# Kernel optimization log

Hardware: AMD Instinct MI355X
Metric: run time of the kernel (lower is better)

Reference implementation:

```python
import jax, jax.numpy as jnp
import numpy as np

N = 100000      # nodes
E = 1600000     # edges (avg degree 16)
IN = 128
HID = 128
HEADS = 4
OUT = 64
NEG_SLOPE = 0.2  # PyG GATv2Conv default


def _normal(key, shape, scale=0.05):
    return scale * jax.random.normal(key, shape, dtype=jnp.float32)


def setup_inputs() -> dict:
    key = jax.random.key(0)
    ks = jax.random.split(key, 20)
    x = jax.random.normal(ks[0], (N, IN), dtype=jnp.float32)
    # edges guaranteed non-self-loop (PyG removes then re-adds self loops)
    src = jax.random.randint(ks[1], (E,), 0, N)
    off = jax.random.randint(ks[2], (E,), 1, N)
    dst = (src + off) % N
    edge_index = jnp.stack([src, dst]).astype(jnp.int64)
    C1 = HID // HEADS  # 32 per head
    return {
        "x": x,
        "edge_index": edge_index,
        # layer 1: GATv2Conv(IN -> C1, heads=HEADS, concat=True)
        "Wl1": _normal(ks[3], (IN, HEADS * C1)), "bl1": jnp.zeros((HEADS * C1,), jnp.float32),
        "Wr1": _normal(ks[4], (IN, HEADS * C1)), "br1": jnp.zeros((HEADS * C1,), jnp.float32),
        "att1": _normal(ks[5], (HEADS, C1)),
        "b1": jnp.zeros((HEADS * C1,), jnp.float32),
        # layer 2: GATv2Conv(HID -> HID, heads=1, concat=False)
        "Wl2": _normal(ks[6], (HID, HID)), "bl2": jnp.zeros((HID,), jnp.float32),
        "Wr2": _normal(ks[7], (HID, HID)), "br2": jnp.zeros((HID,), jnp.float32),
        "att2": _normal(ks[8], (1, HID)),
        "b2": jnp.zeros((HID,), jnp.float32),
        # residual skips
        "skip1_w": _normal(ks[9], (IN, HID)), "skip1_b": jnp.zeros((HID,), jnp.float32),
        "skip2_w": _normal(ks[10], (HID, HID)), "skip2_b": jnp.zeros((HID,), jnp.float32),
        # MLP head
        "mlp1_w": _normal(ks[11], (HID, HID)), "mlp1_b": jnp.zeros((HID,), jnp.float32),
        "mlp2_w": _normal(ks[12], (HID, OUT)), "mlp2_b": jnp.zeros((OUT,), jnp.float32),
    }


def gatv2_layer(x, src, dst, Wl, bl, Wr, br, att, bias, heads, outc, concat, n):
    # x: [n, F]; src/dst: [Etot] (self-loops included)
    xl = (x @ Wl + bl).reshape(n, heads, outc)  # source transform
    xr = (x @ Wr + br).reshape(n, heads, outc)  # target transform
    e = jax.nn.leaky_relu(xl[src] + xr[dst], NEG_SLOPE)   # [Etot, H, C]
    logits = jnp.einsum('ehc,hc->eh', e, att)             # [Etot, H]
    # segment softmax over incoming edges of each target node
    m = jax.ops.segment_max(logits, dst, num_segments=n)
    a = jnp.exp(logits - m[dst])
    denom = jax.ops.segment_sum(a, dst, num_segments=n)
    alpha = a / denom[dst]                                # [Etot, H]
    msg = alpha[:, :, None] * xl[src]                     # [Etot, H, C]
    out = jax.ops.segment_sum(msg, dst, num_segments=n)   # [n, H, C]
    out = out.reshape(n, heads * outc) if concat else out.mean(axis=1)
    return out + bias


def reference(x, edge_index, Wl1, bl1, Wr1, br1, att1, b1,
              Wl2, bl2, Wr2, br2, att2, b2,
              skip1_w, skip1_b, skip2_w, skip2_b,
              mlp1_w, mlp1_b, mlp2_w, mlp2_b):
    n = x.shape[0]
    loop = jnp.arange(n, dtype=edge_index.dtype)
    src = jnp.concatenate([edge_index[0], loop])
    dst = jnp.concatenate([edge_index[1], loop])
    # layer 0 + skip + relu (dropout off: eval mode)
    h = gatv2_layer(x, src, dst, Wl1, bl1, Wr1, br1, att1, b1,
                    HEADS, HID // HEADS, True, n)
    h = jax.nn.relu(h + x @ skip1_w + skip1_b)
    # final conv layer (heads=1, concat=False) + skip
    h2 = gatv2_layer(h, src, dst, Wl2, bl2, Wr2, br2, att2, b2,
                     1, HID, False, n)
    h = h2 + h @ skip2_w + skip2_b
    # MLP head
    out = jax.nn.relu(h @ mlp1_w + mlp1_b) @ mlp2_w + mlp2_b
    return out
```

## Files before the change

### kernel.cpp

```cpp
#include <hip/hip_runtime.h>

#define LEAK 0.2f

typedef __attribute__((ext_vector_type(8))) short short8v;
typedef __attribute__((ext_vector_type(4))) float float4v;

__device__ __forceinline__ ushort f2bf(float f) {
  union { float f; unsigned u; } v; v.f = f;
  unsigned r = v.u + 0x7fffu + ((v.u >> 16) & 1u);
  return (ushort)(r >> 16);
}
__device__ __forceinline__ float bf2f(ushort h) {
  union { unsigned u; float f; } v; v.u = ((unsigned)h) << 16;
  return v.f;
}
__device__ __forceinline__ float lrelu(float t) {
  return fmaf(0.4f, fabsf(t), 0.6f * t);
}

__global__ void count_part(const int* __restrict__ dstp, int* __restrict__ cnt,
                           int E, int N, int nblk) {
  int grp = blockIdx.x & 7;
  int gb = blockIdx.x >> 3;
  int gn = nblk >> 3;
  int lo = (int)(((long long)N * grp) >> 3);
  int hi = (int)(((long long)N * (grp + 1)) >> 3);
  for (int e = gb * blockDim.x + threadIdx.x; e < E; e += gn * blockDim.x) {
    int d = dstp[e];
    if (d >= lo && d < hi) atomicAdd(&cnt[d], 1);
  }
}

__global__ void fill_part(const int* __restrict__ srcp, const int* __restrict__ dstp,
                          const int* __restrict__ rowptr, int* __restrict__ cur,
                          int* __restrict__ csr_src, int E, int N, int nblk) {
  int grp = blockIdx.x & 7;
  int gb = blockIdx.x >> 3;
  int gn = nblk >> 3;
  int lo = (int)(((long long)N * grp) >> 3);
  int hi = (int)(((long long)N * (grp + 1)) >> 3);
  for (int e = gb * blockDim.x + threadIdx.x; e < E; e += gn * blockDim.x) {
    int d = dstp[e];
    if (d >= lo && d < hi) {
      int pos = atomicAdd(&cur[d], 1);
      csr_src[rowptr[d] + pos] = srcp[e];
    }
  }
}

__global__ __launch_bounds__(1024)
void scan_blocks(const int* __restrict__ cnt, int* __restrict__ tscan,
                 int* __restrict__ bsum, int n) {
  __shared__ int sh[1024];
  int t = threadIdx.x;
  int i = blockIdx.x * 1024 + t;
  sh[t] = (i < n) ? cnt[i] + 1 : 0;
  __syncthreads();
  for (int off = 1; off < 1024; off <<= 1) {
    int u = (t >= off) ? sh[t - off] : 0;
    __syncthreads();
    sh[t] += u;
    __syncthreads();
  }
  if (i < n) tscan[i] = sh[t];
  if (t == 1023) bsum[blockIdx.x] = sh[1023];
}

__global__ __launch_bounds__(1024)
void scan_final(int* __restrict__ cnt, const int* __restrict__ tscan,
                const int* __restrict__ bsum, int* __restrict__ rowptr,
                int* __restrict__ csr_src, int n, int nb) {
  __shared__ int sh[1024];
  int t = threadIdx.x;
  sh[t] = (t < nb) ? bsum[t] : 0;
  __syncthreads();
  for (int off = 1; off < 1024; off <<= 1) {
    int u = (t >= off) ? sh[t - off] : 0;
    __syncthreads();
    sh[t] += u;
    __syncthreads();
  }
  int i = blockIdx.x * 1024 + t;
  if (i < n) {
    int bpref = (blockIdx.x == 0) ? 0 : sh[blockIdx.x - 1];
    int incl = bpref + tscan[i];
    rowptr[i] = incl - (cnt[i] + 1);
    csr_src[incl - 1] = i;
    cnt[i] = 0;
  }
  if (blockIdx.x == nb - 1 && t == 0) rowptr[n] = sh[nb - 1];
}

__global__ void split_f32(const float* __restrict__ a, ushort* __restrict__ hi,
                          ushort* __restrict__ lo, int n) {
  int i = (blockIdx.x * blockDim.x + threadIdx.x) * 4;
  if (i >= n) return;
  float4 v = *(const float4*)(a + i);
  ushort h[4], l[4];
  float vv[4] = {v.x, v.y, v.z, v.w};
#pragma unroll
  for (int j = 0; j < 4; ++j) {
    h[j] = f2bf(vv[j]);
    l[j] = f2bf(vv[j] - bf2f(h[j]));
  }
  *(ushort4*)(hi + i) = make_ushort4(h[0], h[1], h[2], h[3]);
  *(ushort4*)(lo + i) = make_ushort4(l[0], l[1], l[2], l[3]);
}

struct PackArgs {
  const float* w[8];
  ushort* o[8];
  int nout[8];
};
__global__ __launch_bounds__(256)
void pack_all(PackArgs pa) {
  int wsel = blockIdx.x >> 3;
  int sub = blockIdx.x & 7;
  const float* W = pa.w[wsel];
  ushort* pk = pa.o[wsel];
  int NOUT = pa.nout[wsel];
  int NT = NOUT / 16;
  int total = NT * 4 * 64;
  int t = sub * 256 + threadIdx.x;
  if (t >= total) return;
  int lane = t & 63;
  int ks = (t >> 6) & 3;
  int nt = t >> 8;
  int col = nt * 16 + (lane & 15);
  int k0 = ks * 32 + (lane >> 4) * 8;
  ushort h[8], l[8];
#pragma unroll
  for (int j = 0; j < 8; ++j) {
    float v = W[(size_t)(k0 + j) * NOUT + col];
    h[j] = f2bf(v);
    l[j] = f2bf(v - bf2f(h[j]));
  }
  size_t fb = ((size_t)(nt * 4 + ks) * 64 + lane) * 8;
  size_t fragsz = (size_t)total * 8;
#pragma unroll
  for (int j = 0; j < 8; ++j) { pk[fb + j] = h[j]; pk[fragsz + fb + j] = l[j]; }
}

__global__ __launch_bounds__(512)
void gemm3_mfma(const ushort* __restrict__ Ahi, const ushort* __restrict__ Alo,
                const ushort* __restrict__ W0, const ushort* __restrict__ W1,
                const ushort* __restrict__ W2,
                const float* __restrict__ b0, const float* __restrict__ b1,
                const float* __restrict__ b2,
                ushort* __restrict__ C0b, ushort* __restrict__ C1b,
                float* __restrict__ C2, int M) {
  int tid = threadIdx.x;
  int w = tid >> 6, lane = tid & 63;
  int l15 = lane & 15, lh = lane >> 4;
  int row0 = blockIdx.x * 64;

  const ushort* Wp[3] = {W0, W1, W2};

  int arow[4];
#pragma unroll
  for (int mt = 0; mt < 4; ++mt) { int rr = row0 + mt * 16 + l15; arow[mt] = rr < M ? rr : M - 1; }

  float4v acc[3][4];
#pragma unroll
  for (int p = 0; p < 3; ++p)
#pragma unroll
    for (int mt = 0; mt < 4; ++mt) {
      acc[p][mt][0] = 0.f; acc[p][mt][1] = 0.f; acc[p][mt][2] = 0.f; acc[p][mt][3] = 0.f;
    }

  const size_t fragsz = (size_t)8 * 4 * 64 * 8;
#pragma unroll 1
  for (int ks = 0; ks < 4; ++ks) {
    short8v bh[3], bl[3];
    size_t fb = ((size_t)(w * 4 + ks) * 64 + lane) * 8;
#pragma unroll
    for (int p = 0; p < 3; ++p) {
      bh[p] = *(const short8v*)(Wp[p] + fb);
      bl[p] = *(const short8v*)(Wp[p] + fragsz + fb);
    }
#pragma unroll
    for (int mt = 0; mt < 4; ++mt) {
      size_t ao = (size_t)arow[mt] * 128 + ks * 32 + lh * 8;
      short8v ah = *(const short8v*)(Ahi + ao);
      short8v al = *(const short8v*)(Alo + ao);
#pragma unroll
      for (int p = 0; p < 3; ++p) {
        acc[p][mt] = __builtin_amdgcn_mfma_f32_16x16x32_bf16(ah, bh[p], acc[p][mt], 0, 0, 0);
        acc[p][mt] = __builtin_amdgcn_mfma_f32_16x16x32_bf16(ah, bl[p], acc[p][mt], 0, 0, 0);
        acc[p][mt] = __builtin_amdgcn_mfma_f32_16x16x32_bf16(al, bh[p], acc[p][mt], 0, 0, 0);
      }
    }
  }

  int col = w * 16 + l15;
  float bb0 = b0[col], bb1 = b1[col], bb2 = b2[col];
#pragma unroll
  for (int mt = 0; mt < 4; ++mt) {
#pragma unroll
    for (int r = 0; r < 4; ++r) {
      int rr = row0 + mt * 16 + lh * 4 + r;
      if (rr < M) {
        C0b[(size_t)rr * 128 + col] = f2bf(acc[0][mt][r] + bb0);
        C1b[(size_t)rr * 128 + col] = f2bf(acc[1][mt][r] + bb1);
        C2[(size_t)rr * 128 + col] = acc[2][mt][r] + bb2;
      }
    }
  }
}

__global__ __launch_bounds__(256)
void mlp_fused(const ushort* __restrict__ Ahi, const ushort* __restrict__ Alo,
               const ushort* __restrict__ W1pk, const float* __restrict__ b1,
               const ushort* __restrict__ W2pk, const float* __restrict__ b2,
               float* __restrict__ out, int M) {
  __shared__ ushort m1[2][16][64][8];
  int tid = threadIdx.x;
  int w = tid >> 6, lane = tid & 63;
  int l15 = lane & 15, lh = lane >> 4;
  int row0 = blockIdx.x * 64;

  int arow[4];
#pragma unroll
  for (int mt = 0; mt < 4; ++mt) { int rr = row0 + mt * 16 + l15; arow[mt] = rr < M ? rr : M - 1; }

  float4v acc1[4][2];
#pragma unroll
  for (int mt = 0; mt < 4; ++mt)
#pragma unroll
    for (int j = 0; j < 2; ++j) {
      acc1[mt][j][0] = 0.f; acc1[mt][j][1] = 0.f; acc1[mt][j][2] = 0.f; acc1[mt][j][3] = 0.f;
    }
  const size_t fragsz1 = (size_t)8 * 4 * 64 * 8;
#pragma unroll 1
  for (int ks = 0; ks < 4; ++ks) {
    short8v bh[2], bl[2];
#pragma unroll
    for (int nt2 = 0; nt2 < 2; ++nt2) {
      size_t fb = ((size_t)((w * 2 + nt2) * 4 + ks) * 64 + lane) * 8;
      bh[nt2] = *(const short8v*)(W1pk + fb);
      bl[nt2] = *(const short8v*)(W1pk + fragsz1 + fb);
    }
#pragma unroll
    for (int mt = 0; mt < 4; ++mt) {
      size_t ao = (size_t)arow[mt] * 128 + ks * 32 + lh * 8;
      short8v ah = *(const short8v*)(Ahi + ao);
      short8v al = *(const short8v*)(Alo + ao);
#pragma unroll
      for (int nt2 = 0; nt2 < 2; ++nt2) {
        acc1[mt][nt2] = __builtin_amdgcn_mfma_f32_16x16x32_bf16(ah, bh[nt2], acc1[mt][nt2], 0, 0, 0);
        acc1[mt][nt2] = __builtin_amdgcn_mfma_f32_16x16x32_bf16(ah, bl[nt2], acc1[mt][nt2], 0, 0, 0);
        acc1[mt][nt2] = __builtin_amdgcn_mfma_f32_16x16x32_bf16(al, bh[nt2], acc1[mt][nt2], 0, 0, 0);
      }
    }
  }
#pragma unroll
  for (int nt2 = 0; nt2 < 2; ++nt2) {
    int col = (w * 2 + nt2) * 16 + l15;
    float bb = b1[col];
    int kf = col >> 3, kr = col & 7;
#pragma unroll
    for (int mt = 0; mt < 4; ++mt) {
#pragma unroll
      for (int r = 0; r < 4; ++r) {
        int row = mt * 16 + lh * 4 + r;
        float v = fmaxf(acc1[mt][nt2][r] + bb, 0.f);
        ushort h = f2bf(v);
        m1[0][kf][row][kr] = h;
        m1[1][kf][row][kr] = f2bf(v - bf2f(h));
      }
    }
  }
  __syncthreads();

  float4v acc2[4];
#pragma unroll
  for (int mt = 0; mt < 4; ++mt) {
    acc2[mt][0] = 0.f; acc2[mt][1] = 0.f; acc2[mt][2] = 0.f; acc2[mt][3] = 0.f;
  }
  const size_t fragsz2 = (size_t)4 * 4 * 64 * 8;
#pragma unroll 1
  for (int ks = 0; ks < 4; ++ks) {
    size_t fb = ((size_t)(w * 4 + ks) * 64 + lane) * 8;
    short8v bh = *(const short8v*)(W2pk + fb);
    short8v bl = *(const short8v*)(W2pk + fragsz2 + fb);
#pragma unroll
    for (int mt = 0; mt < 4; ++mt) {
      int row = mt * 16 + l15;
      short8v ah = *(const short8v*)&m1[0][ks * 4 + lh][row][0];
      short8v al = *(const short8v*)&m1[1][ks * 4 + lh][row][0];
      acc2[mt] = __builtin_amdgcn_mfma_f32_16x16x32_bf16(ah, bh, acc2[mt], 0, 0, 0);
      acc2[mt] = __builtin_amdgcn_mfma_f32_16x16x32_bf16(ah, bl, acc2[mt], 0, 0, 0);
      acc2[mt] = __builtin_amdgcn_mfma_f32_16x16x32_bf16(al, bh, acc2[mt], 0, 0, 0);
    }
  }
  int col = w * 16 + l15;
  float bb = b2[col];
#pragma unroll
  for (int mt = 0; mt < 4; ++mt) {
#pragma unroll
    for (int r = 0; r < 4; ++r) {
      int rr = row0 + mt * 16 + lh * 4 + r;
      if (rr < M) out[(size_t)rr * 64 + col] = acc2[mt][r] + bb;
    }
  }
}

template<int H, bool SPLIT>
__global__ __launch_bounds__(256)
void gat_agg(const ushort* __restrict__ xlb, const ushort* __restrict__ xrb,
             const float* __restrict__ skip, const float* __restrict__ att,
             const float* __restrict__ gbias, const int* __restrict__ rowptr,
             const int* __restrict__ csr_src, float* __restrict__ out,
             ushort* __restrict__ outhi, ushort* __restrict__ outlo,
             int n, int relu) {
  constexpr int GL = (128 / H) / 4;
  int wid = blockIdx.x * (blockDim.x >> 6) + (threadIdx.x >> 6);
  if (wid >= n) return;
  int lane = threadIdx.x & 63;
  int half = lane >> 5;
  int sub = lane & 31;
  size_t base = (size_t)wid * 128 + sub * 4;
  uint2 ur = *(const uint2*)(xrb + base);
  float4 xrv;
  xrv.x = __uint_as_float(ur.x << 16); xrv.y = __uint_as_float(ur.x & 0xFFFF0000u);
  xrv.z = __uint_as_float(ur.y << 16); xrv.w = __uint_as_float(ur.y & 0xFFFF0000u);
  float4 av = *(const float4*)(att + sub * 4);
  float ax = 0.f, ay = 0.f, az = 0.f, aw = 0.f;
  float denom = 0.f;
  int e0 = rowptr[wid], e1 = rowptr[wid + 1];

  int idx = e0 + half;
  for (; idx + 2 < e1; idx += 4) {
    int s0 = csr_src[idx], s1 = csr_src[idx + 2];
    uint2 u0 = *(const uint2*)(xlb + (size_t)s0 * 128 + sub * 4);
    uint2 u1 = *(const uint2*)(xlb + (size_t)s1 * 128 + sub * 4);
    float4 v0, v1;
    v0.x = __uint_as_float(u0.x << 16); v0.y = __uint_as_float(u0.x & 0xFFFF0000u);
    v0.z = __uint_as_float(u0.y << 16); v0.w = __uint_as_float(u0.y & 0xFFFF0000u);
    v1.x = __uint_as_float(u1.x << 16); v1.y = __uint_as_float(u1.x & 0xFFFF0000u);
    v1.z = __uint_as_float(u1.y << 16); v1.w = __uint_as_float(u1.y & 0xFFFF0000u);
    float p0, p1;
    p0 = lrelu(v0.x + xrv.x) * av.x;
    p0 += lrelu(v0.y + xrv.y) * av.y;
    p0 += lrelu(v0.z + xrv.z) * av.z;
    p0 += lrelu(v0.w + xrv.w) * av.w;
    p1 = lrelu(v1.x + xrv.x) * av.x;
    p1 += lrelu(v1.y + xrv.y) * av.y;
    p1 += lrelu(v1.z + xrv.z) * av.z;
    p1 += lrelu(v1.w + xrv.w) * av.w;
#pragma unroll
    for (int o = 1; o < GL; o <<= 1) {
      p0 += __shfl_xor(p0, o, 64);
      p1 += __shfl_xor(p1, o, 64);
    }
    float w0 = __expf(p0), w1 = __expf(p1);
    denom += w0 + w1;
    ax += w0 * v0.x + w1 * v1.x;
    ay += w0 * v0.y + w1 * v1.y;
    az += w0 * v0.z + w1 * v1.z;
    aw += w0 * v0.w + w1 * v1.w;
  }
  for (; idx < e1; idx += 2) {
    int s0 = csr_src[idx];
    uint2 u0 = *(const uint2*)(xlb + (size_t)s0 * 128 + sub * 4);
    float4 v0;
    v0.x = __uint_as_float(u0.x << 16); v0.y = __uint_as_float(u0.x & 0xFFFF0000u);
    v0.z = __uint_as_float(u0.y << 16); v0.w = __uint_as_float(u0.y & 0xFFFF0000u);
    float p0;
    p0 = lrelu(v0.x + xrv.x) * av.x;
    p0 += lrelu(v0.y + xrv.y) * av.y;
    p0 += lrelu(v0.z + xrv.z) * av.z;
    p0 += lrelu(v0.w + xrv.w) * av.w;
#pragma unroll
    for (int o = 1; o < GL; o <<= 1) p0 += __shfl_xor(p0, o, 64);
    float w0 = __expf(p0);
    denom += w0;
    ax += w0 * v0.x;
    ay += w0 * v0.y;
    az += w0 * v0.z;
    aw += w0 * v0.w;
  }

  ax += __shfl_xor(ax, 32, 64);
  ay += __shfl_xor(ay, 32, 64);
  az += __shfl_xor(az, 32, 64);
  aw += __shfl_xor(aw, 32, 64);
  denom += __shfl_xor(denom, 32, 64);

  if (half == 0) {
    float inv = 1.f / denom;
    float4 sk = *(const float4*)(skip + base);
    float4 gb = *(const float4*)(gbias + sub * 4);
    float o0 = ax * inv + gb.x + sk.x;
    float o1 = ay * inv + gb.y + sk.y;
    float o2 = az * inv + gb.z + sk.z;
    float o3 = aw * inv + gb.w + sk.w;
    if (relu) {
      o0 = fmaxf(o0, 0.f); o1 = fmaxf(o1, 0.f);
      o2 = fmaxf(o2, 0.f); o3 = fmaxf(o3, 0.f);
    }
    if (SPLIT) {
      ushort h0 = f2bf(o0), h1 = f2bf(o1), h2 = f2bf(o2), h3 = f2bf(o3);
      *(ushort4*)(outhi + base) = make_ushort4(h0, h1, h2, h3);
      *(ushort4*)(outlo + base) = make_ushort4(f2bf(o0 - bf2f(h0)), f2bf(o1 - bf2f(h1)),
                                               f2bf(o2 - bf2f(h2)), f2bf(o3 - bf2f(h3)));
    } else {
      *(float4*)(out + base) = make_float4(o0, o1, o2, o3);
    }
  }
}

extern "C" void kernel_launch(void* const* d_in, const int* in_sizes, int n_in,
                              void* d_out, int out_size, void* d_ws, size_t ws_size,
                              hipStream_t stream) {
  const float* x       = (const float*)d_in[0];
  const int* ei        = (const int*)d_in[1];
  const float* Wl1     = (const float*)d_in[2];
  const float* bl1     = (const float*)d_in[3];
  const float* Wr1     = (const float*)d_in[4];
  const float* br1     = (const float*)d_in[5];
  const float* att1    = (const float*)d_in[6];
  const float* b1      = (const float*)d_in[7];
  const float* Wl2     = (const float*)d_in[8];
  const float* bl2     = (const float*)d_in[9];
  const float* Wr2     = (const float*)d_in[10];
  const float* br2     = (const float*)d_in[11];
  const float* att2    = (const float*)d_in[12];
  const float* b2      = (const float*)d_in[13];
  const float* skip1_w = (const float*)d_in[14];
  const float* skip1_b = (const float*)d_in[15];
  const float* skip2_w = (const float*)d_in[16];
  const float* skip2_b = (const float*)d_in[17];
  const float* mlp1_w  = (const float*)d_in[18];
  const float* mlp1_b  = (const float*)d_in[19];
  const float* mlp2_w  = (const float*)d_in[20];
  const float* mlp2_b  = (const float*)d_in[21];

  const int N = in_sizes[0] / 128;
  const int E = in_sizes[1] / 2;
  float* out = (float*)d_out;

  char* ws = (char*)d_ws;
  size_t off = 0;
  auto alloc = [&](size_t bytes) -> void* {
    void* p = ws + off;
    off = (off + bytes + 255) & ~(size_t)255;
    return p;
  };
  int* rowptr  = (int*)alloc((size_t)(N + 1) * sizeof(int));
  int* cnt     = (int*)alloc((size_t)N * sizeof(int));
  int* tscan   = (int*)alloc((size_t)N * sizeof(int));
  int* bsum    = (int*)alloc((size_t)1024 * sizeof(int));
  int* csr_src = (int*)alloc((size_t)(E + N) * sizeof(int));
  ushort* wpk[8];
  for (int i = 0; i < 8; ++i) wpk[i] = (ushort*)alloc(128 * 128 * 2 * sizeof(ushort));
  ushort* p0hi = (ushort*)alloc((size_t)N * 128 * sizeof(ushort));
  ushort* p0lo = (ushort*)alloc((size_t)N * 128 * sizeof(ushort));
  ushort* xlb  = (ushort*)alloc((size_t)N * 128 * sizeof(ushort));
  ushort* xrb  = (ushort*)alloc((size_t)N * 128 * sizeof(ushort));
  float* bufC  = (float*)alloc((size_t)N * 128 * sizeof(float));

  const int* srcp = ei;
  const int* dstp = ei + E;

  const int ggrid = (N + 63) / 64;
  const int agrid = (N + 3) / 4;
  const int nb = (N + 1023) / 1024;
  const int PARTB = 2048;

  hipMemsetAsync(cnt, 0, (size_t)N * sizeof(int), stream);
  count_part<<<PARTB, 256, 0, stream>>>(dstp, cnt, E, N, PARTB);
  scan_blocks<<<nb, 1024, 0, stream>>>(cnt, tscan, bsum, N);
  scan_final<<<nb, 1024, 0, stream>>>(cnt, tscan, bsum, rowptr, csr_src, N, nb);
  fill_part<<<PARTB, 256, 0, stream>>>(srcp, dstp, rowptr, cnt, csr_src, E, N, PARTB);

  PackArgs pa;
  pa.w[0] = Wl1;    pa.o[0] = wpk[0]; pa.nout[0] = 128;
  pa.w[1] = Wr1;    pa.o[1] = wpk[1]; pa.nout[1] = 128;
  pa.w[2] = skip1_w;pa.o[2] = wpk[2]; pa.nout[2] = 128;
  pa.w[3] = Wl2;    pa.o[3] = wpk[3]; pa.nout[3] = 128;
  pa.w[4] = Wr2;    pa.o[4] = wpk[4]; pa.nout[4] = 128;
  pa.w[5] = skip2_w;pa.o[5] = wpk[5]; pa.nout[5] = 128;
  pa.w[6] = mlp1_w; pa.o[6] = wpk[6]; pa.nout[6] = 128;
  pa.w[7] = mlp2_w; pa.o[7] = wpk[7]; pa.nout[7] = 64;
  pack_all<<<64, 256, 0, stream>>>(pa);
  split_f32<<<(N * 128 / 4 + 255) / 256, 256, 0, stream>>>(x, p0hi, p0lo, N * 128);

  gemm3_mfma<<<ggrid, 512, 0, stream>>>(p0hi, p0lo, wpk[0], wpk[1], wpk[2],
                                        bl1, br1, skip1_b, xlb, xrb, bufC, N);
  gat_agg<4, true><<<agrid, 256, 0, stream>>>(xlb, xrb, bufC, att1, b1,
                                              rowptr, csr_src, nullptr, p0hi, p0lo, N, 1);

  gemm3_mfma<<<ggrid, 512, 0, stream>>>(p0hi, p0lo, wpk[3], wpk[4], wpk[5],
                                        bl2, br2, skip2_b, xlb, xrb, bufC, N);
  gat_agg<1, true><<<agrid, 256, 0, stream>>>(xlb, xrb, bufC, att2, b2,
                                              rowptr, csr_src, nullptr, p0hi, p0lo, N, 0);

  mlp_fused<<<ggrid, 256, 0, stream>>>(p0hi, p0lo, wpk[6], mlp1_b, wpk[7], mlp2_b, out, N);
}
```

Baseline: 552.0 us.

## Split leaky-relu attention into linear per-node dots and fuse input split into GEMM

Uses lrelu(t)=0.6t+0.4|t| to move the linear part of the attention logit out of the edge loop. A new dot_att kernel precomputes att·xl and att·xr per node, so each edge only needs the abs term plus two scalar loads. The first-layer GEMM now reads fp32 x directly and splits it into bf16 hi/lo in-register, which removes the separate split_f32 pass and its hi/lo write and read. In exchange there are two extra small kernels and per-edge gathers from the dl array.

```diff
diff --git a/kernel.cpp b/kernel.cpp
--- a/kernel.cpp
+++ b/kernel.cpp
@@ -1,6 +1,4 @@
 #include <hip/hip_runtime.h>
-
-#define LEAK 0.2f
 
 typedef __attribute__((ext_vector_type(8))) short short8v;
 typedef __attribute__((ext_vector_type(4))) float float4v;
@@ -14,8 +12,8 @@
   union { unsigned u; float f; } v; v.u = ((unsigned)h) << 16;
   return v.f;
 }
-__device__ __forceinline__ float lrelu(float t) {
-  return fmaf(0.4f, fabsf(t), 0.6f * t);
+__device__ __forceinline__ float ubf(unsigned u, int hi) {
+  return __uint_as_float(hi ? (u & 0xFFFF0000u) : (u << 16));
 }
 
 __global__ void count_part(const int* __restrict__ dstp, int* __restrict__ cnt,
@@ -89,22 +87,6 @@
     cnt[i] = 0;
   }
   if (blockIdx.x == nb - 1 && t == 0) rowptr[n] = sh[nb - 1];
-}
-
-__global__ void split_f32(const float* __restrict__ a, ushort* __restrict__ hi,
-                          ushort* __restrict__ lo, int n) {
-  int i = (blockIdx.x * blockDim.x + threadIdx.x) * 4;
-  if (i >= n) return;
-  float4 v = *(const float4*)(a + i);
-  ushort h[4], l[4];
-  float vv[4] = {v.x, v.y, v.z, v.w};
-#pragma unroll
-  for (int j = 0; j < 4; ++j) {
-    h[j] = f2bf(vv[j]);
-    l[j] = f2bf(vv[j] - bf2f(h[j]));
-  }
-  *(ushort4*)(hi + i) = make_ushort4(h[0], h[1], h[2], h[3]);
-  *(ushort4*)(lo + i) = make_ushort4(l[0], l[1], l[2], l[3]);
 }
 
 struct PackArgs {
@@ -141,8 +123,9 @@
   for (int j = 0; j < 8; ++j) { pk[fb + j] = h[j]; pk[fragsz + fb + j] = l[j]; }
 }
 
+template<bool AF32>
 __global__ __launch_bounds__(512)
-void gemm3_mfma(const ushort* __restrict__ Ahi, const ushort* __restrict__ Alo,
+void gemm3_mfma(const void* __restrict__ A1, const void* __restrict__ A2,
                 const ushort* __restrict__ W0, const ushort* __restrict__ W1,
                 const ushort* __restrict__ W2,
                 const float* __restrict__ b0, const float* __restrict__ b1,
@@ -181,8 +164,22 @@
 #pragma unroll
     for (int mt = 0; mt < 4; ++mt) {
       size_t ao = (size_t)arow[mt] * 128 + ks * 32 + lh * 8;
-      short8v ah = *(const short8v*)(Ahi + ao);
-      short8v al = *(const short8v*)(Alo + ao);
+      short8v ah, al;
+      if constexpr (AF32) {
+        const float* Af = (const float*)A1;
+        float4 f0 = *(const float4*)(Af + ao);
+        float4 f1 = *(const float4*)(Af + ao + 4);
+        float fv[8] = {f0.x, f0.y, f0.z, f0.w, f1.x, f1.y, f1.z, f1.w};
+#pragma unroll
+        for (int j = 0; j < 8; ++j) {
+          ushort h = f2bf(fv[j]);
+          ah[j] = (short)h;
+          al[j] = (short)f2bf(fv[j] - bf2f(h));
+        }
+      } else {
+        ah = *(const short8v*)((const ushort*)A1 + ao);
+        al = *(const short8v*)((const ushort*)A2 + ao);
+      }
 #pragma unroll
       for (int p = 0; p < 3; ++p) {
         acc[p][mt] = __builtin_amdgcn_mfma_f32_16x16x32_bf16(ah, bh[p], acc[p][mt], 0, 0, 0);
@@ -205,6 +202,33 @@
         C2[(size_t)rr * 128 + col] = acc[2][mt][r] + bb2;
       }
     }
+  }
+}
+
+template<int H>
+__global__ __launch_bounds__(256)
+void dot_att(const ushort* __restrict__ xlb, const ushort* __restrict__ xrb,
+             const float* __restrict__ att, float* __restrict__ dl,
+             float* __restrict__ dr, int n) {
+  constexpr int RL = (H == 4) ? 16 : 64;
+  int wid = blockIdx.x * 4 + (threadIdx.x >> 6);
+  if (wid >= n) return;
+  int lane = threadIdx.x & 63;
+  size_t base = (size_t)wid * 128 + lane * 2;
+  float a0 = att[lane * 2], a1 = att[lane * 2 + 1];
+  unsigned ul = *(const unsigned*)(xlb + base);
+  unsigned ur = *(const unsigned*)(xrb + base);
+  float pl = fmaf(a1, ubf(ul, 1), a0 * ubf(ul, 0));
+  float pr = fmaf(a1, ubf(ur, 1), a0 * ubf(ur, 0));
+#pragma unroll
+  for (int o = 1; o < RL; o <<= 1) {
+    pl += __shfl_xor(pl, o, 64);
+    pr += __shfl_xor(pr, o, 64);
+  }
+  if ((lane & (RL - 1)) == 0) {
+    int h = lane / RL;
+    dl[(size_t)wid * H + h] = pl;
+    dr[(size_t)wid * H + h] = pr;
   }
 }
 
@@ -309,22 +333,26 @@
 __global__ __launch_bounds__(256)
 void gat_agg(const ushort* __restrict__ xlb, const ushort* __restrict__ xrb,
              const float* __restrict__ skip, const float* __restrict__ att,
+             const float* __restrict__ dl, const float* __restrict__ dr,
              const float* __restrict__ gbias, const int* __restrict__ rowptr,
              const int* __restrict__ csr_src, float* __restrict__ out,
              ushort* __restrict__ outhi, ushort* __restrict__ outlo,
              int n, int relu) {
   constexpr int GL = (128 / H) / 4;
+  constexpr int HS = (H == 4) ? 3 : 5;
   int wid = blockIdx.x * (blockDim.x >> 6) + (threadIdx.x >> 6);
   if (wid >= n) return;
   int lane = threadIdx.x & 63;
   int half = lane >> 5;
   int sub = lane & 31;
+  int head = sub >> HS;
   size_t base = (size_t)wid * 128 + sub * 4;
   uint2 ur = *(const uint2*)(xrb + base);
   float4 xrv;
-  xrv.x = __uint_as_float(ur.x << 16); xrv.y = __uint_as_float(ur.x & 0xFFFF0000u);
-  xrv.z = __uint_as_float(ur.y << 16); xrv.w = __uint_as_float(ur.y & 0xFFFF0000u);
+  xrv.x = ubf(ur.x, 0); xrv.y = ubf(ur.x, 1);
+  xrv.z = ubf(ur.y, 0); xrv.w = ubf(ur.y, 1);
   float4 av = *(const float4*)(att + sub * 4);
+  float drd = dr[(size_t)wid * H + head];
   float ax = 0.f, ay = 0.f, az = 0.f, aw = 0.f;
   float denom = 0.f;
   int e0 = rowptr[wid], e1 = rowptr[wid + 1];
@@ -332,28 +360,29 @@
   int idx = e0 + half;
   for (; idx + 2 < e1; idx += 4) {
     int s0 = csr_src[idx], s1 = csr_src[idx + 2];
+    float dls0 = dl[(size_t)s0 * H + head];
+    float dls1 = dl[(size_t)s1 * H + head];
     uint2 u0 = *(const uint2*)(xlb + (size_t)s0 * 128 + sub * 4);
     uint2 u1 = *(const uint2*)(xlb + (size_t)s1 * 128 + sub * 4);
     float4 v0, v1;
-    v0.x = __uint_as_float(u0.x << 16); v0.y = __uint_as_float(u0.x & 0xFFFF0000u);
-    v0.z = __uint_as_float(u0.y << 16); v0.w = __uint_as_float(u0.y & 0xFFFF0000u);
-    v1.x = __uint_as_float(u1.x << 16); v1.y = __uint_as_float(u1.x & 0xFFFF0000u);
-    v1.z = __uint_as_float(u1.y << 16); v1.w = __uint_as_float(u1.y & 0xFFFF0000u);
+    v0.x = ubf(u0.x, 0); v0.y = ubf(u0.x, 1); v0.z = ubf(u0.y, 0); v0.w = ubf(u0.y, 1);
+    v1.x = ubf(u1.x, 0); v1.y = ubf(u1.x, 1); v1.z = ubf(u1.y, 0); v1.w = ubf(u1.y, 1);
     float p0, p1;
-    p0 = lrelu(v0.x + xrv.x) * av.x;
-    p0 += lrelu(v0.y + xrv.y) * av.y;
-    p0 += lrelu(v0.z + xrv.z) * av.z;
-    p0 += lrelu(v0.w + xrv.w) * av.w;
-    p1 = lrelu(v1.x + xrv.x) * av.x;
-    p1 += lrelu(v1.y + xrv.y) * av.y;
-    p1 += lrelu(v1.z + xrv.z) * av.z;
-    p1 += lrelu(v1.w + xrv.w) * av.w;
+    p0 = av.x * fabsf(v0.x + xrv.x);
+    p0 = fmaf(av.y, fabsf(v0.y + xrv.y), p0);
+    p0 = fmaf(av.z, fabsf(v0.z + xrv.z), p0);
+    p0 = fmaf(av.w, fabsf(v0.w + xrv.w), p0);
+    p1 = av.x * fabsf(v1.x + xrv.x);
+    p1 = fmaf(av.y, fabsf(v1.y + xrv.y), p1);
+    p1 = fmaf(av.z, fabsf(v1.z + xrv.z), p1);
+    p1 = fmaf(av.w, fabsf(v1.w + xrv.w), p1);
 #pragma unroll
     for (int o = 1; o < GL; o <<= 1) {
       p0 += __shfl_xor(p0, o, 64);
       p1 += __shfl_xor(p1, o, 64);
     }
-    float w0 = __expf(p0), w1 = __expf(p1);
+    float w0 = __expf(fmaf(0.4f, p0, 0.6f * (dls0 + drd)));
+    float w1 = __expf(fmaf(0.4f, p1, 0.6f * (dls1 + drd)));
     denom += w0 + w1;
     ax += w0 * v0.x + w1 * v1.x;
     ay += w0 * v0.y + w1 * v1.y;
@@ -362,18 +391,18 @@
   }
   for (; idx < e1; idx += 2) {
     int s0 = csr_src[idx];
+    float dls0 = dl[(size_t)s0 * H + head];
     uint2 u0 = *(const uint2*)(xlb + (size_t)s0 * 128 + sub * 4);
     float4 v0;
-    v0.x = __uint_as_float(u0.x << 16); v0.y = __uint_as_float(u0.x & 0xFFFF0000u);
-    v0.z = __uint_as_float(u0.y << 16); v0.w = __uint_as_float(u0.y & 0xFFFF0000u);
+    v0.x = ubf(u0.x, 0); v0.y = ubf(u0.x, 1); v0.z = ubf(u0.y, 0); v0.w = ubf(u0.y, 1);
     float p0;
-    p0 = lrelu(v0.x + xrv.x) * av.x;
-    p0 += lrelu(v0.y + xrv.y) * av.y;
-    p0 += lrelu(v0.z + xrv.z) * av.z;
-    p0 += lrelu(v0.w + xrv.w) * av.w;
+    p0 = av.x * fabsf(v0.x + xrv.x);
+    p0 = fmaf(av.y, fabsf(v0.y + xrv.y), p0);
+    p0 = fmaf(av.z, fabsf(v0.z + xrv.z), p0);
+    p0 = fmaf(av.w, fabsf(v0.w + xrv.w), p0);
 #pragma unroll
     for (int o = 1; o < GL; o <<= 1) p0 += __shfl_xor(p0, o, 64);
-    float w0 = __expf(p0);
+    float w0 = __expf(fmaf(0.4f, p0, 0.6f * (dls0 + drd)));
     denom += w0;
     ax += w0 * v0.x;
     ay += w0 * v0.y;
@@ -459,6 +488,8 @@
   ushort* xlb  = (ushort*)alloc((size_t)N * 128 * sizeof(ushort));
   ushort* xrb  = (ushort*)alloc((size_t)N * 128 * sizeof(ushort));
   float* bufC  = (float*)alloc((size_t)N * 128 * sizeof(float));
+  float* dl    = (float*)alloc((size_t)N * 4 * sizeof(float));
+  float* dr    = (float*)alloc((size_t)N * 4 * sizeof(float));
 
   const int* srcp = ei;
   const int* dstp = ei + E;
@@ -484,16 +515,19 @@
   pa.w[6] = mlp1_w; pa.o[6] = wpk[6]; pa.nout[6] = 128;
   pa.w[7] = mlp2_w; pa.o[7] = wpk[7]; pa.nout[7] = 64;
   pack_all<<<64, 256, 0, stream>>>(pa);
-  split_f32<<<(N * 128 / 4 + 255) / 256, 256, 0, stream>>>(x, p0hi, p0lo, N * 128);
-
-  gemm3_mfma<<<ggrid, 512, 0, stream>>>(p0hi, p0lo, wpk[0], wpk[1], wpk[2],
-                                        bl1, br1, skip1_b, xlb, xrb, bufC, N);
-  gat_agg<4, true><<<agrid, 256, 0, stream>>>(xlb, xrb, bufC, att1, b1,
+
+  gemm3_mfma<true><<<ggrid, 512, 0, stream>>>((const void*)x, nullptr,
+                                              wpk[0], wpk[1], wpk[2],
+                                              bl1, br1, skip1_b, xlb, xrb, bufC, N);
+  dot_att<4><<<agrid, 256, 0, stream>>>(xlb, xrb, att1, dl, dr, N);
+  gat_agg<4, true><<<agrid, 256, 0, stream>>>(xlb, xrb, bufC, att1, dl, dr, b1,
                                               rowptr, csr_src, nullptr, p0hi, p0lo, N, 1);
 
-  gemm3_mfma<<<ggrid, 512, 0, stream>>>(p0hi, p0lo, wpk[3], wpk[4], wpk[5],
-                                        bl2, br2, skip2_b, xlb, xrb, bufC, N);
-  gat_agg<1, true><<<agrid, 256, 0, stream>>>(xlb, xrb, bufC, att2, b2,
+  gemm3_mfma<false><<<ggrid, 512, 0, stream>>>((const void*)p0hi, (const void*)p0lo,
+                                               wpk[3], wpk[4], wpk[5],
+                                               bl2, br2, skip2_b, xlb, xrb, bufC, N);
+  dot_att<1><<<agrid, 256, 0, stream>>>(xlb, xrb, att2, dl, dr, N);
+  gat_agg<1, true><<<agrid, 256, 0, stream>>>(xlb, xrb, bufC, att2, dl, dr, b2,
                                               rowptr, csr_src, nullptr, p0hi, p0lo, N, 0);
 
   mlp_fused<<<ggrid, 256, 0, stream>>>(p0hi, p0lo, wpk[6], mlp1_b, wpk[7], mlp2_b, out, N);
```

Result: slower. 573.1 us (+3.8%).
